# Performance work log

Hardware: AMD Instinct MI355X
Metric: run time of the kernel (lower is better)

Reference implementation:

```python
import jax, jax.numpy as jnp
import numpy as np

N_NODES = 100000
N_EDGES = 1600000
DIM = 64
BN_EPS = 1e-5


def setup_inputs() -> dict:
    key = jax.random.key(0)
    ks = jax.random.split(key, 6)
    x = jax.random.normal(ks[0], (N_NODES, DIM), dtype=jnp.float32)
    edge_index = jax.random.randint(ks[1], (2, N_EDGES), 0, N_NODES, dtype=jnp.int32)
    W = jax.random.normal(ks[2], (DIM, DIM), dtype=jnp.float32) / np.sqrt(DIM)
    b = jax.random.normal(ks[3], (DIM,), dtype=jnp.float32) * 0.01
    gamma = jnp.ones((DIM,), dtype=jnp.float32)
    beta = jnp.zeros((DIM,), dtype=jnp.float32)
    return {"x": x, "edge_index": edge_index, "W": W, "b": b, "gamma": gamma, "beta": beta}


def reference(x, edge_index, W, b, gamma, beta):
    n = x.shape[0]
    src, dst = edge_index[0], edge_index[1]
    # GCNConv adds self loops
    loop = jnp.arange(n, dtype=edge_index.dtype)
    src = jnp.concatenate([src, loop])
    dst = jnp.concatenate([dst, loop])
    # symmetric degree normalization: D^-1/2 (A+I) D^-1/2
    deg = jax.ops.segment_sum(jnp.ones(src.shape[0], x.dtype), dst, num_segments=n)
    dinv = jnp.where(deg > 0, jax.lax.rsqrt(deg), 0.0)
    norm = dinv[src] * dinv[dst]  # [E+N]
    h = x @ W  # [N, D] transform before aggregation (GCN order)
    msg = h[src] * norm[:, None]  # gather + scale
    out = jax.ops.segment_sum(msg, dst, num_segments=n) + b  # scatter-add
    # BatchNorm1d (training mode: batch statistics, biased variance)
    mean = jnp.mean(out, axis=0)
    var = jnp.mean(jnp.square(out - mean), axis=0)
    out = (out - mean) * jax.lax.rsqrt(var + BN_EPS) * gamma + beta
    # ReLU; dropout is identity in eval mode
    return jax.nn.relu(out)
```

## Files before the change

kernel.cpp:

```cpp
#include <hip/hip_runtime.h>

#define N_NODES 100000
#define N_EDGES 1600000
#define DIM 64
#define BN_EPS 1e-5f

#define BNODES 128
#define NBUCK ((N_NODES + BNODES - 1) / BNODES)
#define CAP_RAW 2560
#define CAP_OUT 3584
#define TILE 2048
#define ABLK ((N_EDGES + TILE - 1) / TILE)

#define GBLK 6250
#define NREP 32

typedef __bf16 bf16x8 __attribute__((ext_vector_type(8)));
typedef float floatx4 __attribute__((ext_vector_type(4)));

static __device__ __forceinline__ unsigned short f2bf(float f) {
    unsigned u = __float_as_uint(f);
    u = (u + 0x7FFFu + ((u >> 16) & 1u)) >> 16;
    return (unsigned short)u;
}
static __device__ __forceinline__ float bf2f(unsigned short h) {
    return __uint_as_float(((unsigned)h) << 16);
}

__global__ void __launch_bounds__(512)
passA_kernel(const int* __restrict__ src, const int* __restrict__ dst,
             int* __restrict__ cur, unsigned int* __restrict__ entries, int E) {
    __shared__ int hist[NBUCK];
    __shared__ int lbase[NBUCK];
    int t = threadIdx.x;
    for (int i = t; i < NBUCK; i += 512) hist[i] = 0;
    __syncthreads();

    int e0   = blockIdx.x * TILE;
    int eend = min(e0 + TILE, E);
    int eb   = e0 + t * 4;

    int dreg[4], sreg[4], ne = 0;
    if (eb + 3 < eend) {
        int4 d4 = *(const int4*)(dst + eb);
        int4 s4 = *(const int4*)(src + eb);
        dreg[0] = d4.x; dreg[1] = d4.y; dreg[2] = d4.z; dreg[3] = d4.w;
        sreg[0] = s4.x; sreg[1] = s4.y; sreg[2] = s4.z; sreg[3] = s4.w;
        ne = 4;
    } else {
        for (int e = eb; e < eend && ne < 4; ++e, ++ne) {
            dreg[ne] = dst[e];
            sreg[ne] = src[e];
        }
    }
#pragma unroll
    for (int k = 0; k < 4; ++k)
        if (k < ne) atomicAdd(&hist[dreg[k] >> 7], 1);
    __syncthreads();
    for (int i = t; i < NBUCK; i += 512) {
        int ii = i + (blockIdx.x * 331) % NBUCK;
        if (ii >= NBUCK) ii -= NBUCK;
        int c = hist[ii];
        lbase[ii] = (c > 0) ? atomicAdd(&cur[ii], c) : 0;
        hist[ii] = 0;
    }
    __syncthreads();
#pragma unroll
    for (int k = 0; k < 4; ++k) {
        if (k >= ne) break;
        int s = sreg[k];
        int d = dreg[k];
        int b = d >> 7;
        int r = atomicAdd(&hist[b], 1);
        int pos = lbase[b] + r;
        if (pos < CAP_RAW)
            entries[(size_t)b * CAP_OUT + pos] = ((unsigned)s << 7) | (unsigned)(d & 127);
    }
}

__global__ void __launch_bounds__(256)
build_sort_kernel(unsigned int* __restrict__ entries, const int* __restrict__ cur,
                  int* __restrict__ rowbeg, int* __restrict__ rowend,
                  float* __restrict__ dinv, int dummyIdx, int N) {
    __shared__ int hist[BNODES * 4];
    __shared__ int nstart[BNODES];
    __shared__ int cursor[BNODES * 4];
    __shared__ int w0tot;
    int bucket = blockIdx.x;
    int t = threadIdx.x;
    int lane = t & 63, wv = t >> 6;
    int node0 = bucket * BNODES;
    int nn = min(BNODES, N - node0);
    int cnt = min(cur[bucket], CAP_RAW);
    unsigned int* eb = entries + (size_t)bucket * CAP_OUT;

    for (int i = t; i < BNODES * 4; i += 256) hist[i] = 0;
    __syncthreads();

    unsigned int ereg[10];
#pragma unroll
    for (int k = 0; k < 10; ++k) {
        int i = t + k * 256;
        if (i < cnt) {
            unsigned int e = eb[i];
            ereg[k] = e;
            int s = (int)(e >> 7);
            int q = (s >= 25000) + (s >= 50000) + (s >= 75000);
            atomicAdd(&hist[((e & 127) << 2) | q], 1);
        }
    }
    __syncthreads();

    int deg_t = 0, pdeg_t = 0;
    if (t < BNODES) {
        deg_t = hist[t * 4] + hist[t * 4 + 1] + hist[t * 4 + 2] + hist[t * 4 + 3];
        pdeg_t = (deg_t + 7) & ~7;
    }
    int v = pdeg_t;
#pragma unroll
    for (int off = 1; off < 64; off <<= 1) {
        int u = __shfl_up(v, off, 64);
        if (lane >= off) v += u;
    }
    if (t == 63) w0tot = v;
    __syncthreads();
    if (t < BNODES) {
        int incl = v + (wv == 1 ? w0tot : 0);
        int ex = incl - pdeg_t;
        nstart[t] = ex;
        int o = ex;
        cursor[t * 4 + 0] = o; o += hist[t * 4 + 0];
        cursor[t * 4 + 1] = o; o += hist[t * 4 + 1];
        cursor[t * 4 + 2] = o; o += hist[t * 4 + 2];
        cursor[t * 4 + 3] = o;
    }
    __syncthreads();
#pragma unroll
    for (int k = 0; k < 10; ++k) {
        int i = t + k * 256;
        if (i < cnt) {
            unsigned int e = ereg[k];
            int s = (int)(e >> 7);
            int q = (s >= 25000) + (s >= 50000) + (s >= 75000);
            int p = atomicAdd(&cursor[((e & 127) << 2) | q], 1);
            eb[p] = (unsigned)s;
        }
    }
    if (t < nn) {
        int dg  = deg_t;
        int pdg = pdeg_t;
        int base = nstart[t];
        for (int k = dg; k < pdg; ++k) eb[base + k] = (unsigned)dummyIdx;
        int gbase = bucket * CAP_OUT + base;
        rowbeg[node0 + t] = gbase;
        rowend[node0 + t] = gbase + pdg;
        dinv[node0 + t] = rsqrtf((float)(dg + 1));
    }
}

__global__ void __launch_bounds__(256)
gemm_kernel(const float* __restrict__ x, const float* __restrict__ W,
            const float* __restrict__ dinv, unsigned short* __restrict__ hb, int N) {
    int t = threadIdx.x;
    int lane = t & 63, wv = t >> 6;
    int m = lane & 15, quad = lane >> 4;
    int row0 = blockIdx.x * 64 + wv * 16;
    if (row0 >= N) return;

    bf16x8 bfrag[2][4];
#pragma unroll
    for (int c = 0; c < 2; ++c)
#pragma unroll
        for (int nt = 0; nt < 4; ++nt) {
            bf16x8 f;
#pragma unroll
            for (int j = 0; j < 8; ++j) {
                int k = c * 32 + quad * 8 + j;
                f[j] = (__bf16)W[k * DIM + nt * 16 + m];
            }
            bfrag[c][nt] = f;
        }

    const float* xr = x + (size_t)(row0 + m) * DIM;
    bf16x8 afrag[2];
#pragma unroll
    for (int c = 0; c < 2; ++c) {
        float4 lo = *(const float4*)(xr + c * 32 + quad * 8);
        float4 hi = *(const float4*)(xr + c * 32 + quad * 8 + 4);
        bf16x8 f;
        f[0] = (__bf16)lo.x; f[1] = (__bf16)lo.y; f[2] = (__bf16)lo.z; f[3] = (__bf16)lo.w;
        f[4] = (__bf16)hi.x; f[5] = (__bf16)hi.y; f[6] = (__bf16)hi.z; f[7] = (__bf16)hi.w;
        afrag[c] = f;
    }
    float dv = dinv[row0 + m];
#pragma unroll
    for (int nt = 0; nt < 4; ++nt) {
        floatx4 acc = {0.f, 0.f, 0.f, 0.f};
        acc = __builtin_amdgcn_mfma_f32_16x16x32_bf16(bfrag[0][nt], afrag[0], acc, 0, 0, 0);
        acc = __builtin_amdgcn_mfma_f32_16x16x32_bf16(bfrag[1][nt], afrag[1], acc, 0, 0, 0);
        ushort4 pk;
        pk.x = f2bf(acc[0] * dv);
        pk.y = f2bf(acc[1] * dv);
        pk.z = f2bf(acc[2] * dv);
        pk.w = f2bf(acc[3] * dv);
        *(ushort4*)(hb + (size_t)(row0 + m) * DIM + nt * 16 + quad * 4) = pk;
    }
}

__global__ void __launch_bounds__(256)
gather_kernel(const int* __restrict__ rowbeg, const int* __restrict__ rowend,
              const unsigned int* __restrict__ srt, const unsigned short* __restrict__ hb,
              const float* __restrict__ dinv, unsigned short* __restrict__ hbout,
              float* __restrict__ gstatRep, int N) {
    __shared__ float red[2][4][64];
    int lane = threadIdx.x & 63;
    int wv   = threadIdx.x >> 6;
    int g    = blockIdx.x * 4 + wv;
    int n0   = g << 2;
    float s_sum = 0.f, s_sq = 0.f;

    if (n0 < N) {
        int beg = __builtin_amdgcn_readfirstlane(rowbeg[n0]);
        int s1  = __builtin_amdgcn_readfirstlane(rowbeg[n0 + 1]);
        int s2  = __builtin_amdgcn_readfirstlane(rowbeg[n0 + 2]);
        int s3  = __builtin_amdgcn_readfirstlane(rowbeg[n0 + 3]);
        int end = __builtin_amdgcn_readfirstlane(rowend[n0 + 3]);
        float acc0 = 0.f, acc1 = 0.f, acc2 = 0.f, acc3 = 0.f;

        unsigned int sv = (beg + lane < end) ? srt[beg + lane] : 0u;
        for (int base = beg; base < end; base += 64) {
            int nidx = base + 64 + lane;
            unsigned int sv_next = (nidx < end) ? srt[nidx] : 0u;
            int cn = min(64, end - base);
            int j = 0;
            for (; j + 16 <= cn; j += 16) {
                int pA = base + j;
                int pB = pA + 8;
                int kA = (pA >= s1) + (pA >= s2) + (pA >= s3);
                int kB = (pB >= s1) + (pB >= s2) + (pB >= s3);
                float v[16];
#pragma unroll
                for (int u = 0; u < 16; ++u) {
                    unsigned int s = (unsigned)__builtin_amdgcn_readlane((int)sv, j + u);
                    v[u] = bf2f(hb[(size_t)s * DIM + lane]);
                }
                float cA = ((v[0] + v[1]) + (v[2] + v[3])) +
                           ((v[4] + v[5]) + (v[6] + v[7]));
                float cB = ((v[8] + v[9]) + (v[10] + v[11])) +
                           ((v[12] + v[13]) + (v[14] + v[15]));
                acc0 += (kA == 0) ? cA : 0.f;
                acc1 += (kA == 1) ? cA : 0.f;
                acc2 += (kA == 2) ? cA : 0.f;
                acc3 += (kA == 3) ? cA : 0.f;
                acc0 += (kB == 0) ? cB : 0.f;
                acc1 += (kB == 1) ? cB : 0.f;
                acc2 += (kB == 2) ? cB : 0.f;
                acc3 += (kB == 3) ? cB : 0.f;
            }
            for (; j < cn; j += 8) {
                int p0 = base + j;
                int k = (p0 >= s1) + (p0 >= s2) + (p0 >= s3);
                float v[8];
#pragma unroll
                for (int u = 0; u < 8; ++u) {
                    unsigned int s = (unsigned)__builtin_amdgcn_readlane((int)sv, j + u);
                    v[u] = bf2f(hb[(size_t)s * DIM + lane]);
                }
                float csum = ((v[0] + v[1]) + (v[2] + v[3])) +
                             ((v[4] + v[5]) + (v[6] + v[7]));
                acc0 += (k == 0) ? csum : 0.f;
                acc1 += (k == 1) ? csum : 0.f;
                acc2 += (k == 2) ? csum : 0.f;
                acc3 += (k == 3) ? csum : 0.f;
            }
            sv = sv_next;
        }

        float v0 = (acc0 + bf2f(hb[(size_t)(n0 + 0) * DIM + lane])) * dinv[n0 + 0];
        float v1 = (acc1 + bf2f(hb[(size_t)(n0 + 1) * DIM + lane])) * dinv[n0 + 1];
        float v2 = (acc2 + bf2f(hb[(size_t)(n0 + 2) * DIM + lane])) * dinv[n0 + 2];
        float v3 = (acc3 + bf2f(hb[(size_t)(n0 + 3) * DIM + lane])) * dinv[n0 + 3];
        unsigned short r0 = f2bf(v0), r1 = f2bf(v1), r2 = f2bf(v2), r3 = f2bf(v3);
        hbout[(size_t)(n0 + 0) * DIM + lane] = r0;
        hbout[(size_t)(n0 + 1) * DIM + lane] = r1;
        hbout[(size_t)(n0 + 2) * DIM + lane] = r2;
        hbout[(size_t)(n0 + 3) * DIM + lane] = r3;
        float w0 = bf2f(r0), w1 = bf2f(r1), w2 = bf2f(r2), w3 = bf2f(r3);
        s_sum = ((w0 + w1) + (w2 + w3));
        s_sq  = ((w0 * w0 + w1 * w1) + (w2 * w2 + w3 * w3));
    }

    red[0][wv][lane] = s_sum;
    red[1][wv][lane] = s_sq;
    __syncthreads();
    if (threadIdx.x < 128) {
        int c = threadIdx.x & 63;
        int which = threadIdx.x >> 6;
        float v = red[which][0][c] + red[which][1][c] + red[which][2][c] + red[which][3][c];
        float* dst = gstatRep + (size_t)(blockIdx.x & (NREP - 1)) * 128 + which * 64 + c;
        atomicAdd(dst, v);
    }
}

__global__ void __launch_bounds__(256)
finish_kernel(const ushort4* __restrict__ hbo, float4* __restrict__ out,
              const float* __restrict__ gstatRep,
              const float* __restrict__ gamma, const float* __restrict__ beta,
              int total4, int N) {
    __shared__ float scale[64];
    __shared__ float shift[64];
    __shared__ float stat[128];
    int t = threadIdx.x;
    if (t < 128) {
        int c = t & 63;
        int which = t >> 6;
        float acc = 0.f;
#pragma unroll
        for (int r = 0; r < NREP; ++r)
            acc += gstatRep[(size_t)r * 128 + which * 64 + c];
        stat[t] = acc;
    }
    __syncthreads();
    if (t < 64) {
        float invN = 1.0f / (float)N;
        float mean = stat[t] * invN;
        float var  = stat[64 + t] * invN - mean * mean;
        float sc   = gamma[t] * rsqrtf(var + BN_EPS);
        scale[t] = sc;
        shift[t] = beta[t] - mean * sc;
    }
    __syncthreads();
    int i = blockIdx.x * blockDim.x + t;
    if (i >= total4) return;
    int c = (i * 4) & 63;
    ushort4 u = hbo[i];
    float4 v;
    float a0 = fmaf(bf2f(u.x), scale[c],     shift[c]);
    float a1 = fmaf(bf2f(u.y), scale[c + 1], shift[c + 1]);
    float a2 = fmaf(bf2f(u.z), scale[c + 2], shift[c + 2]);
    float a3 = fmaf(bf2f(u.w), scale[c + 3], shift[c + 3]);
    v.x = a0 > 0.f ? a0 : 0.f;
    v.y = a1 > 0.f ? a1 : 0.f;
    v.z = a2 > 0.f ? a2 : 0.f;
    v.w = a3 > 0.f ? a3 : 0.f;
    out[i] = v;
}

extern "C" void kernel_launch(void* const* d_in, const int* in_sizes, int n_in,
                              void* d_out, int out_size, void* d_ws, size_t ws_size,
                              hipStream_t stream) {
    const float* x     = (const float*)d_in[0];
    const int*   eidx  = (const int*)d_in[1];
    const float* W     = (const float*)d_in[2];
    const float* gamma = (const float*)d_in[4];
    const float* beta  = (const float*)d_in[5];
    float* out = (float*)d_out;

    const int N = N_NODES;
    const int total = N * DIM;

    const int* src = eidx;
    const int* dst = eidx + N_EDGES;

    char* ws = (char*)d_ws;
    size_t off_hb      = 0;
    size_t off_hbout   = off_hb + (size_t)N * DIM * 2;
    size_t off_dinv    = off_hbout + (size_t)N * DIM * 2;
    size_t off_rowbeg  = off_dinv + (size_t)N * 4;
    size_t off_rowend  = off_rowbeg + (size_t)N * 4;
    size_t off_entries = off_rowend + (size_t)N * 4;
    size_t off_z       = off_entries + (size_t)NBUCK * CAP_OUT * 4;

    unsigned short* hb     = (unsigned short*)(ws + off_hb);
    unsigned short* hbout  = (unsigned short*)(ws + off_hbout);
    float*          dinv   = (float*)(ws + off_dinv);
    int*            rowbeg = (int*)(ws + off_rowbeg);
    int*            rowend = (int*)(ws + off_rowend);
    unsigned int*   entries = (unsigned int*)(ws + off_entries);
    int*   cur      = (int*)(ws + off_z + 128);
    float* gstatRep = (float*)(cur + NBUCK);
    int dummyIdx = (int)(off_z / (DIM * 2));

    size_t zbytes = 128 + (size_t)NBUCK * 4 + (size_t)NREP * 128 * 4;
    hipMemsetAsync(ws + off_z, 0, zbytes, stream);

    passA_kernel<<<ABLK, 512, 0, stream>>>(src, dst, cur, entries, N_EDGES);

    build_sort_kernel<<<NBUCK, 256, 0, stream>>>(entries, cur, rowbeg, rowend, dinv,
                                                 dummyIdx, N);

    gemm_kernel<<<(N + 63) / 64, 256, 0, stream>>>(x, W, dinv, hb, N);

    gather_kernel<<<GBLK, 256, 0, stream>>>(rowbeg, rowend, entries, hb, dinv,
                                            hbout, gstatRep, N);

    finish_kernel<<<(total / 4 + 255) / 256, 256, 0, stream>>>((const ushort4*)hbout,
                                                               (float4*)out, gstatRep,
                                                               gamma, beta, total / 4, N);
}
```

Before: 183.6 us.

## Fuse feature GEMM into edge bucketing kernel and apply source norm in gather

Removes the standalone GEMM launch by computing x@W inside the edge bucketing pass, with each block's waves handling 16-row tiles. The bucketing pass grows to 1024 threads and 4096 edges per block so its wave count covers all rows. Because dinv is not yet known when the fused GEMM runs, the source-side normalization moves into the gather loop as a per-edge readlane and FMA on a prefetched dinv value. This adds ALU and readlane work in the gather and enlarges the fused kernel's register footprint.

```diff
diff --git a/kernel.cpp b/kernel.cpp
--- a/kernel.cpp
+++ b/kernel.cpp
@@ -9,7 +9,7 @@
 #define NBUCK ((N_NODES + BNODES - 1) / BNODES)
 #define CAP_RAW 2560
 #define CAP_OUT 3584
-#define TILE 2048
+#define TILE 4096
 #define ABLK ((N_EDGES + TILE - 1) / TILE)
 
 #define GBLK 6250
@@ -27,13 +27,15 @@
     return __uint_as_float(((unsigned)h) << 16);
 }
 
-__global__ void __launch_bounds__(512)
+__global__ void __launch_bounds__(1024, 8)
 passA_kernel(const int* __restrict__ src, const int* __restrict__ dst,
-             int* __restrict__ cur, unsigned int* __restrict__ entries, int E) {
+             int* __restrict__ cur, unsigned int* __restrict__ entries,
+             const float* __restrict__ x, const float* __restrict__ W,
+             unsigned short* __restrict__ hb, int E) {
     __shared__ int hist[NBUCK];
     __shared__ int lbase[NBUCK];
     int t = threadIdx.x;
-    for (int i = t; i < NBUCK; i += 512) hist[i] = 0;
+    if (t < NBUCK) hist[t] = 0;
     __syncthreads();
 
     int e0   = blockIdx.x * TILE;
@@ -57,8 +59,8 @@
     for (int k = 0; k < 4; ++k)
         if (k < ne) atomicAdd(&hist[dreg[k] >> 7], 1);
     __syncthreads();
-    for (int i = t; i < NBUCK; i += 512) {
-        int ii = i + (blockIdx.x * 331) % NBUCK;
+    if (t < NBUCK) {
+        int ii = t + (blockIdx.x * 331) % NBUCK;
         if (ii >= NBUCK) ii -= NBUCK;
         int c = hist[ii];
         lbase[ii] = (c > 0) ? atomicAdd(&cur[ii], c) : 0;
@@ -75,6 +77,49 @@
         int pos = lbase[b] + r;
         if (pos < CAP_RAW)
             entries[(size_t)b * CAP_OUT + pos] = ((unsigned)s << 7) | (unsigned)(d & 127);
+    }
+
+    int w = blockIdx.x * 16 + (t >> 6);
+    if (w < N_NODES / 16) {
+        int lane = t & 63;
+        int m = lane & 15, quad = lane >> 4;
+        int row = w * 16 + m;
+        bf16x8 bfrag[2][4];
+#pragma unroll
+        for (int c = 0; c < 2; ++c)
+#pragma unroll
+            for (int nt = 0; nt < 4; ++nt) {
+                bf16x8 f;
+#pragma unroll
+                for (int j = 0; j < 8; ++j) {
+                    int k = c * 32 + quad * 8 + j;
+                    f[j] = (__bf16)W[k * DIM + nt * 16 + m];
+                }
+                bfrag[c][nt] = f;
+            }
+        const float* xr = x + (size_t)row * DIM;
+        bf16x8 afrag[2];
+#pragma unroll
+        for (int c = 0; c < 2; ++c) {
+            float4 lo = *(const float4*)(xr + c * 32 + quad * 8);
+            float4 hi = *(const float4*)(xr + c * 32 + quad * 8 + 4);
+            bf16x8 f;
+            f[0] = (__bf16)lo.x; f[1] = (__bf16)lo.y; f[2] = (__bf16)lo.z; f[3] = (__bf16)lo.w;
+            f[4] = (__bf16)hi.x; f[5] = (__bf16)hi.y; f[6] = (__bf16)hi.z; f[7] = (__bf16)hi.w;
+            afrag[c] = f;
+        }
+#pragma unroll
+        for (int nt = 0; nt < 4; ++nt) {
+            floatx4 acc = {0.f, 0.f, 0.f, 0.f};
+            acc = __builtin_amdgcn_mfma_f32_16x16x32_bf16(bfrag[0][nt], afrag[0], acc, 0, 0, 0);
+            acc = __builtin_amdgcn_mfma_f32_16x16x32_bf16(bfrag[1][nt], afrag[1], acc, 0, 0, 0);
+            ushort4 pk;
+            pk.x = f2bf(acc[0]);
+            pk.y = f2bf(acc[1]);
+            pk.z = f2bf(acc[2]);
+            pk.w = f2bf(acc[3]);
+            *(ushort4*)(hb + (size_t)row * DIM + nt * 16 + quad * 4) = pk;
+        }
     }
 }
 
@@ -159,55 +204,6 @@
 }
 
 __global__ void __launch_bounds__(256)
-gemm_kernel(const float* __restrict__ x, const float* __restrict__ W,
-            const float* __restrict__ dinv, unsigned short* __restrict__ hb, int N) {
-    int t = threadIdx.x;
-    int lane = t & 63, wv = t >> 6;
-    int m = lane & 15, quad = lane >> 4;
-    int row0 = blockIdx.x * 64 + wv * 16;
-    if (row0 >= N) return;
-
-    bf16x8 bfrag[2][4];
-#pragma unroll
-    for (int c = 0; c < 2; ++c)
-#pragma unroll
-        for (int nt = 0; nt < 4; ++nt) {
-            bf16x8 f;
-#pragma unroll
-            for (int j = 0; j < 8; ++j) {
-                int k = c * 32 + quad * 8 + j;
-                f[j] = (__bf16)W[k * DIM + nt * 16 + m];
-            }
-            bfrag[c][nt] = f;
-        }
-
-    const float* xr = x + (size_t)(row0 + m) * DIM;
-    bf16x8 afrag[2];
-#pragma unroll
-    for (int c = 0; c < 2; ++c) {
-        float4 lo = *(const float4*)(xr + c * 32 + quad * 8);
-        float4 hi = *(const float4*)(xr + c * 32 + quad * 8 + 4);
-        bf16x8 f;
-        f[0] = (__bf16)lo.x; f[1] = (__bf16)lo.y; f[2] = (__bf16)lo.z; f[3] = (__bf16)lo.w;
-        f[4] = (__bf16)hi.x; f[5] = (__bf16)hi.y; f[6] = (__bf16)hi.z; f[7] = (__bf16)hi.w;
-        afrag[c] = f;
-    }
-    float dv = dinv[row0 + m];
-#pragma unroll
-    for (int nt = 0; nt < 4; ++nt) {
-        floatx4 acc = {0.f, 0.f, 0.f, 0.f};
-        acc = __builtin_amdgcn_mfma_f32_16x16x32_bf16(bfrag[0][nt], afrag[0], acc, 0, 0, 0);
-        acc = __builtin_amdgcn_mfma_f32_16x16x32_bf16(bfrag[1][nt], afrag[1], acc, 0, 0, 0);
-        ushort4 pk;
-        pk.x = f2bf(acc[0] * dv);
-        pk.y = f2bf(acc[1] * dv);
-        pk.z = f2bf(acc[2] * dv);
-        pk.w = f2bf(acc[3] * dv);
-        *(ushort4*)(hb + (size_t)(row0 + m) * DIM + nt * 16 + quad * 4) = pk;
-    }
-}
-
-__global__ void __launch_bounds__(256)
 gather_kernel(const int* __restrict__ rowbeg, const int* __restrict__ rowend,
               const unsigned int* __restrict__ srt, const unsigned short* __restrict__ hb,
               const float* __restrict__ dinv, unsigned short* __restrict__ hbout,
@@ -228,9 +224,12 @@
         float acc0 = 0.f, acc1 = 0.f, acc2 = 0.f, acc3 = 0.f;
 
         unsigned int sv = (beg + lane < end) ? srt[beg + lane] : 0u;
+        float dv_l = dinv[min((int)sv, N_NODES - 1)];
+#define DLN(u) __uint_as_float((unsigned)__builtin_amdgcn_readlane(__float_as_int(dv_l), j + (u)))
         for (int base = beg; base < end; base += 64) {
             int nidx = base + 64 + lane;
             unsigned int sv_next = (nidx < end) ? srt[nidx] : 0u;
+            float dv_next = dinv[min((int)sv_next, N_NODES - 1)];
             int cn = min(64, end - base);
             int j = 0;
             for (; j + 16 <= cn; j += 16) {
@@ -244,10 +243,14 @@
                     unsigned int s = (unsigned)__builtin_amdgcn_readlane((int)sv, j + u);
                     v[u] = bf2f(hb[(size_t)s * DIM + lane]);
                 }
-                float cA = ((v[0] + v[1]) + (v[2] + v[3])) +
-                           ((v[4] + v[5]) + (v[6] + v[7]));
-                float cB = ((v[8] + v[9]) + (v[10] + v[11])) +
-                           ((v[12] + v[13]) + (v[14] + v[15]));
+                float cA = (fmaf(DLN(0), v[0], DLN(1) * v[1]) +
+                            fmaf(DLN(2), v[2], DLN(3) * v[3])) +
+                           (fmaf(DLN(4), v[4], DLN(5) * v[5]) +
+                            fmaf(DLN(6), v[6], DLN(7) * v[7]));
+                float cB = (fmaf(DLN(8), v[8], DLN(9) * v[9]) +
+                            fmaf(DLN(10), v[10], DLN(11) * v[11])) +
+                           (fmaf(DLN(12), v[12], DLN(13) * v[13]) +
+                            fmaf(DLN(14), v[14], DLN(15) * v[15]));
                 acc0 += (kA == 0) ? cA : 0.f;
                 acc1 += (kA == 1) ? cA : 0.f;
                 acc2 += (kA == 2) ? cA : 0.f;
@@ -266,20 +269,25 @@
                     unsigned int s = (unsigned)__builtin_amdgcn_readlane((int)sv, j + u);
                     v[u] = bf2f(hb[(size_t)s * DIM + lane]);
                 }
-                float csum = ((v[0] + v[1]) + (v[2] + v[3])) +
-                             ((v[4] + v[5]) + (v[6] + v[7]));
+                float csum = (fmaf(DLN(0), v[0], DLN(1) * v[1]) +
+                              fmaf(DLN(2), v[2], DLN(3) * v[3])) +
+                             (fmaf(DLN(4), v[4], DLN(5) * v[5]) +
+                              fmaf(DLN(6), v[6], DLN(7) * v[7]));
                 acc0 += (k == 0) ? csum : 0.f;
                 acc1 += (k == 1) ? csum : 0.f;
                 acc2 += (k == 2) ? csum : 0.f;
                 acc3 += (k == 3) ? csum : 0.f;
             }
             sv = sv_next;
-        }
-
-        float v0 = (acc0 + bf2f(hb[(size_t)(n0 + 0) * DIM + lane])) * dinv[n0 + 0];
-        float v1 = (acc1 + bf2f(hb[(size_t)(n0 + 1) * DIM + lane])) * dinv[n0 + 1];
-        float v2 = (acc2 + bf2f(hb[(size_t)(n0 + 2) * DIM + lane])) * dinv[n0 + 2];
-        float v3 = (acc3 + bf2f(hb[(size_t)(n0 + 3) * DIM + lane])) * dinv[n0 + 3];
+            dv_l = dv_next;
+        }
+#undef DLN
+
+        float d0 = dinv[n0 + 0], d1 = dinv[n0 + 1], d2 = dinv[n0 + 2], d3 = dinv[n0 + 3];
+        float v0 = (acc0 + bf2f(hb[(size_t)(n0 + 0) * DIM + lane]) * d0) * d0;
+        float v1 = (acc1 + bf2f(hb[(size_t)(n0 + 1) * DIM + lane]) * d1) * d1;
+        float v2 = (acc2 + bf2f(hb[(size_t)(n0 + 2) * DIM + lane]) * d2) * d2;
+        float v3 = (acc3 + bf2f(hb[(size_t)(n0 + 3) * DIM + lane]) * d3) * d3;
         unsigned short r0 = f2bf(v0), r1 = f2bf(v1), r2 = f2bf(v2), r3 = f2bf(v3);
         hbout[(size_t)(n0 + 0) * DIM + lane] = r0;
         hbout[(size_t)(n0 + 1) * DIM + lane] = r1;
@@ -384,12 +392,10 @@
     size_t zbytes = 128 + (size_t)NBUCK * 4 + (size_t)NREP * 128 * 4;
     hipMemsetAsync(ws + off_z, 0, zbytes, stream);
 
-    passA_kernel<<<ABLK, 512, 0, stream>>>(src, dst, cur, entries, N_EDGES);
+    passA_kernel<<<ABLK, 1024, 0, stream>>>(src, dst, cur, entries, x, W, hb, N_EDGES);
 
     build_sort_kernel<<<NBUCK, 256, 0, stream>>>(entries, cur, rowbeg, rowend, dinv,
                                                  dummyIdx, N);
-
-    gemm_kernel<<<(N + 63) / 64, 256, 0, stream>>>(x, W, dinv, hb, N);
 
     gather_kernel<<<GBLK, 256, 0, stream>>>(rowbeg, rowend, entries, hb, dinv,
                                             hbout, gstatRep, N);
```

After: 194.9 us. +6.2%, slower.
